# Optimization experiments

Measured on AMD Instinct MI355X. Metric: run time of the kernel, lower is better.

The kernel has to match this reference:

```python
import jax, jax.numpy as jnp
import numpy as np

N_NODES = 100000
N_EDGES = 1600000
D = 128
NEG_SLOPE = 0.01  # torch F.leaky_relu default


def setup_inputs() -> dict:
    key = jax.random.key(0)
    k1, k2, k3, k4, k5, k6 = jax.random.split(key, 6)
    input = jax.random.normal(k1, (N_NODES, D), dtype=jnp.float32)
    edge_row = jax.random.randint(k2, (N_EDGES,), 0, N_NODES, dtype=jnp.int32)
    edge_col = jax.random.randint(k3, (N_EDGES,), 0, N_NODES, dtype=jnp.int32)
    edge_val = jax.random.uniform(k4, (N_EDGES,), dtype=jnp.float32)
    # learned params: W1: Linear(D, D, bias=False), W2: Linear(2D, D, bias=False)
    # torch stores weight as [out, in]; apply as x @ W.T
    bound1 = 1.0 / np.sqrt(D)
    bound2 = 1.0 / np.sqrt(2 * D)
    W1 = jax.random.uniform(k5, (D, D), dtype=jnp.float32, minval=-bound1, maxval=bound1)
    W2 = jax.random.uniform(k6, (D, 2 * D), dtype=jnp.float32, minval=-bound2, maxval=bound2)
    return {"input": input, "edge_row": edge_row, "edge_col": edge_col,
            "edge_val": edge_val, "W1": W1, "W2": W2}


def reference(input, edge_row, edge_col, edge_val, W1, W2):
    # proj_input = W1(input)
    proj = input @ W1.T                                   # [N, D]
    # neighboor = spmm(adj, proj): out[i] = sum_e val[e] * proj[col[e]] for row[e]==i
    msg = edge_val[:, None] * proj[edge_col]              # [E, D]
    neigh = jax.ops.segment_sum(msg, edge_row, num_segments=input.shape[0])  # [N, D]
    h = jnp.concatenate([input + neigh, input * neigh], axis=-1)  # [N, 2D]
    return jax.nn.leaky_relu(h @ W2.T, NEG_SLOPE)         # [N, D]
```

## Files before the change

kernel.cpp:

```cpp
#include <hip/hip_runtime.h>

#define DIM 128
#define BROWS 128
#define BCAP 3072
#define BK_EDGES 2048

typedef __attribute__((ext_vector_type(8))) short short8;
typedef __attribute__((ext_vector_type(4))) float f32x4;

__device__ __forceinline__ unsigned short f2bf(float f) {
    unsigned u = __float_as_uint(f);
    u += 0x7fffu + ((u >> 16) & 1u);
    return (unsigned short)(u >> 16);
}
__device__ __forceinline__ float bf2f(unsigned short b) {
    return __uint_as_float(((unsigned)b) << 16);
}

__global__ void k_pre(const float4* __restrict__ in, const float* __restrict__ W1,
                      const float* __restrict__ W2, unsigned short* __restrict__ inputb,
                      unsigned short* __restrict__ w1b, unsigned short* __restrict__ w2b,
                      int* __restrict__ gcur, int n4, int nCvt, int nbuk) {
    int b = blockIdx.x;
    if (b < nCvt) {
        int i = b * 256 + threadIdx.x;
        if (i < n4) {
            float4 v = in[i];
            *(ushort4*)(inputb + (long)i * 4) =
                make_ushort4(f2bf(v.x), f2bf(v.y), f2bf(v.z), f2bf(v.w));
        }
    } else if (b < nCvt + 192) {
        int idx = (b - nCvt) * 256 + threadIdx.x;
        if (idx < 16384)      w1b[idx] = f2bf(W1[idx]);
        else                  w2b[idx - 16384] = f2bf(W2[idx - 16384]);
    } else {
        int i = (b - nCvt - 192) * 256 + threadIdx.x;
        if (i < nbuk) gcur[i] = 0;
    }
}

__global__ __launch_bounds__(256) void k_bucket(const int* __restrict__ er,
                                                const int* __restrict__ ec,
                                                const float* __restrict__ ev,
                                                int* __restrict__ gcur,
                                                int2* __restrict__ edata, int E, int nbuk) {
    __shared__ int lhist[800];
    __shared__ int lpos[800];
    for (int b = threadIdx.x; b < nbuk; b += 256) lhist[b] = 0;
    __syncthreads();
    int e0 = blockIdx.x * BK_EDGES;
    for (int j = 0; j < BK_EDGES; j += 256) {
        int e = e0 + j + threadIdx.x;
        if (e < E) atomicAdd(&lhist[er[e] >> 7], 1);
    }
    __syncthreads();
    for (int b = threadIdx.x; b < nbuk; b += 256) {
        int c = lhist[b];
        int g = (c > 0) ? atomicAdd(&gcur[b], c) : 0;
        lpos[b] = b * BCAP + g;
    }
    __syncthreads();
    for (int j = 0; j < BK_EDGES; j += 256) {
        int e = e0 + j + threadIdx.x;
        if (e < E) {
            int r = er[e], b = r >> 7;
            int p = atomicAdd(&lpos[b], 1);
            if (p < (b + 1) * BCAP)
                edata[p] = make_int2(((r & 127) << 17) | ec[e], __float_as_int(ev[e]));
        }
    }
}

__global__ __launch_bounds__(256) void k_csr(int2* __restrict__ edata,
                                             const int* __restrict__ gcur,
                                             int* __restrict__ rs, int* __restrict__ re) {
    __shared__ int2 sed[BCAP];
    __shared__ int hist[BROWS];
    __shared__ int scan[BROWS];
    __shared__ int lcur[BROWS];
    int b = blockIdx.x, tid = threadIdx.x;
    int cnt = gcur[b]; if (cnt > BCAP) cnt = BCAP;
    int2* ed = edata + (long)b * BCAP;
    if (tid < BROWS) hist[tid] = 0;
    for (int i = tid; i < cnt; i += 256) sed[i] = ed[i];
    __syncthreads();
    for (int i = tid; i < cnt; i += 256) atomicAdd(&hist[sed[i].x >> 17], 1);
    __syncthreads();
    if (tid < BROWS) scan[tid] = hist[tid];
    __syncthreads();
    for (int off = 1; off < BROWS; off <<= 1) {
        int v = (tid < BROWS && tid >= off) ? scan[tid - off] : 0;
        __syncthreads();
        if (tid < BROWS) scan[tid] += v;
        __syncthreads();
    }
    if (tid < BROWS) {
        int excl = scan[tid] - hist[tid];
        lcur[tid] = excl;
        int row = b * BROWS + tid;
        rs[row] = b * BCAP + excl;
        re[row] = b * BCAP + excl + hist[tid];
    }
    __syncthreads();
    for (int i = tid; i < cnt; i += 256) {
        int2 v = sed[i];
        int p = atomicAdd(&lcur[v.x >> 17], 1);
        ed[p] = make_int2(v.x & 0x1FFFF, v.y);
    }
}

__global__ __launch_bounds__(256) void k_gather(const unsigned short* __restrict__ xb,
                                                const int2* __restrict__ edata,
                                                const int* __restrict__ rs,
                                                const int* __restrict__ re,
                                                unsigned short* __restrict__ aggb, int N) {
    int wave = threadIdx.x >> 6, lane = threadIdx.x & 63;
    int row = blockIdx.x * 4 + wave;
    if (row >= N) return;
    int beg = rs[row], end = re[row];
    float accx = 0.f, accy = 0.f;
    const unsigned* xw = (const unsigned*)xb;
    for (int p = beg; p < end; p += 64) {
        int nc = end - p; if (nc > 64) nc = 64;
        int2 ed = (lane < nc) ? edata[p + lane] : make_int2(0, 0);
        int j = 0;
        for (; j + 4 <= nc; j += 4) {
            int c0 = __shfl(ed.x, j),     c1 = __shfl(ed.x, j + 1);
            int c2 = __shfl(ed.x, j + 2), c3 = __shfl(ed.x, j + 3);
            float v0 = __int_as_float(__shfl(ed.y, j));
            float v1 = __int_as_float(__shfl(ed.y, j + 1));
            float v2 = __int_as_float(__shfl(ed.y, j + 2));
            float v3 = __int_as_float(__shfl(ed.y, j + 3));
            unsigned u0 = xw[(long)c0 * 64 + lane];
            unsigned u1 = xw[(long)c1 * 64 + lane];
            unsigned u2 = xw[(long)c2 * 64 + lane];
            unsigned u3 = xw[(long)c3 * 64 + lane];
            accx += v0 * __uint_as_float(u0 << 16);
            accy += v0 * __uint_as_float(u0 & 0xffff0000u);
            accx += v1 * __uint_as_float(u1 << 16);
            accy += v1 * __uint_as_float(u1 & 0xffff0000u);
            accx += v2 * __uint_as_float(u2 << 16);
            accy += v2 * __uint_as_float(u2 & 0xffff0000u);
            accx += v3 * __uint_as_float(u3 << 16);
            accy += v3 * __uint_as_float(u3 & 0xffff0000u);
        }
        for (; j < nc; ++j) {
            int c = __shfl(ed.x, j);
            float v = __int_as_float(__shfl(ed.y, j));
            unsigned u = xw[(long)c * 64 + lane];
            accx += v * __uint_as_float(u << 16);
            accy += v * __uint_as_float(u & 0xffff0000u);
        }
    }
    *(ushort2*)(aggb + (long)row * DIM + lane * 2) = make_ushort2(f2bf(accx), f2bf(accy));
}

__global__ __launch_bounds__(256, 4) void k_fused(const unsigned short* __restrict__ aggb,
                                                  const unsigned short* __restrict__ inputb,
                                                  const unsigned short* __restrict__ w1b,
                                                  const unsigned short* __restrict__ w2b,
                                                  float* __restrict__ out, int N) {
    __shared__ __align__(16) unsigned short sh[2 * 64 * 136];
    int w = threadIdx.x >> 6, lane = threadIdx.x & 63;
    int quad = lane >> 4, lq = lane & 15;
    int blk0 = blockIdx.x * 64;
    unsigned short* sh0 = sh;
    unsigned short* sh1 = sh + 64 * 136;

    short8 b1[2][4];
#pragma unroll
    for (int ntl = 0; ntl < 2; ++ntl)
#pragma unroll
        for (int kb = 0; kb < 4; ++kb)
            b1[ntl][kb] = *(const short8*)(w1b + ((w * 2 + ntl) * 16 + lq) * DIM +
                                           kb * 32 + quad * 8);

#pragma unroll
    for (int mt = 0; mt < 4; ++mt) {
        short8 afr[4];
        {
            int row = blk0 + mt * 16 + lq; if (row >= N) row = N - 1;
#pragma unroll
            for (int kb = 0; kb < 4; ++kb)
                afr[kb] = *(const short8*)(aggb + (long)row * DIM + kb * 32 + quad * 8);
        }
#pragma unroll
        for (int ntl = 0; ntl < 2; ++ntl) {
            f32x4 c = {0.f, 0.f, 0.f, 0.f};
#pragma unroll
            for (int kb = 0; kb < 4; ++kb)
                c = __builtin_amdgcn_mfma_f32_16x16x32_bf16(afr[kb], b1[ntl][kb], c, 0, 0, 0);
            int nt = w * 2 + ntl;
#pragma unroll
            for (int rg = 0; rg < 4; ++rg) {
                int r = blk0 + mt * 16 + quad * 4 + rg;
                int rr = (r < N) ? r : (N - 1);
                float x = bf2f(inputb[(long)rr * DIM + nt * 16 + lq]);
                float nb = c[rg];
                int off = (mt * 16 + quad * 4 + rg) * 136 + nt * 16 + lq;
                sh0[off] = f2bf(x + nb);
                sh1[off] = f2bf(x * nb);
            }
        }
    }

    short8 b2[2][8];
#pragma unroll
    for (int ntl = 0; ntl < 2; ++ntl)
#pragma unroll
        for (int kb = 0; kb < 8; ++kb)
            b2[ntl][kb] = *(const short8*)(w2b + ((w * 2 + ntl) * 16 + lq) * 256 +
                                           kb * 32 + quad * 8);
    __syncthreads();

#pragma unroll
    for (int mt = 0; mt < 4; ++mt) {
        int arow = (mt * 16 + lq) * 136;
        short8 a0[4], a1[4];
#pragma unroll
        for (int kb = 0; kb < 4; ++kb) {
            a0[kb] = *(const short8*)(sh0 + arow + kb * 32 + quad * 8);
            a1[kb] = *(const short8*)(sh1 + arow + kb * 32 + quad * 8);
        }
#pragma unroll
        for (int ntl = 0; ntl < 2; ++ntl) {
            f32x4 c = {0.f, 0.f, 0.f, 0.f};
#pragma unroll
            for (int kb = 0; kb < 4; ++kb)
                c = __builtin_amdgcn_mfma_f32_16x16x32_bf16(a0[kb], b2[ntl][kb], c, 0, 0, 0);
#pragma unroll
            for (int kb = 0; kb < 4; ++kb)
                c = __builtin_amdgcn_mfma_f32_16x16x32_bf16(a1[kb], b2[ntl][kb + 4], c, 0, 0, 0);
            int nt = w * 2 + ntl;
#pragma unroll
            for (int rg = 0; rg < 4; ++rg) {
                int r = blk0 + mt * 16 + quad * 4 + rg;
                if (r < N) {
                    float v = c[rg];
                    v = (v > 0.f) ? v : 0.01f * v;
                    out[(long)r * DIM + nt * 16 + lq] = v;
                }
            }
        }
    }
}

extern "C" void kernel_launch(void* const* d_in, const int* in_sizes, int n_in,
                              void* d_out, int out_size, void* d_ws, size_t ws_size,
                              hipStream_t stream) {
    const float* input = (const float*)d_in[0];
    const int*   er    = (const int*)d_in[1];
    const int*   ec    = (const int*)d_in[2];
    const float* ev    = (const float*)d_in[3];
    const float* W1    = (const float*)d_in[4];
    const float* W2    = (const float*)d_in[5];
    int N = in_sizes[0] / DIM;
    int E = in_sizes[1];
    float* out = (float*)d_out;
    int nbuk = (N + BROWS - 1) / BROWS;

    int* ws = (int*)d_ws;
    int* gcur = ws;
    int2* edata = (int2*)(ws + 1024);
    int* rs = (int*)(edata + (long)nbuk * BCAP);
    int* re = rs + (long)nbuk * BROWS;
    unsigned short* w1b = (unsigned short*)(re + (long)nbuk * BROWS);
    unsigned short* w2b = w1b + 16384;
    unsigned short* inputb = w2b + 32768;
    unsigned short* aggb = inputb + (long)N * DIM;

    int n4 = N * (DIM / 4);
    int nCvt = (n4 + 255) / 256;
    int nZero = (nbuk + 255) / 256;
    k_pre<<<nCvt + 192 + nZero, 256, 0, stream>>>(
        (const float4*)input, W1, W2, inputb, w1b, w2b, gcur, n4, nCvt, nbuk);

    k_bucket<<<(E + BK_EDGES - 1) / BK_EDGES, 256, 0, stream>>>(
        er, ec, ev, gcur, edata, E, nbuk);

    k_csr<<<nbuk, 256, 0, stream>>>(edata, gcur, rs, re);

    k_gather<<<(N + 3) / 4, 256, 0, stream>>>(inputb, edata, rs, re, aggb, N);

    k_fused<<<(N + 63) / 64, 256, 0, stream>>>(aggb, inputb, w1b, w2b, out, N);
}
```

Measured before the change: 279.9 us.

## Split gather wave into 8 edge groups with 16-byte loads and shuffle reduction

The per-row gather now splits each 64-lane wave into 8 groups of 8 lanes. Each group handles a different edge and loads the full bf16 row with two 16-byte vector loads per lane, instead of one 4-byte load per lane over edges processed one after another. Partial sums are combined with xor-shuffles at the end, and one group writes the result with vector stores. This is meant to raise memory-level parallelism and cut per-edge shuffle overhead. In exchange it uses more registers, adds a reduction step, and leaves groups idle on rows with few or non-multiple-of-8 edges.

```diff
diff --git a/kernel.cpp b/kernel.cpp
--- a/kernel.cpp
+++ b/kernel.cpp
@@ -118,41 +118,46 @@
     int row = blockIdx.x * 4 + wave;
     if (row >= N) return;
     int beg = rs[row], end = re[row];
-    float accx = 0.f, accy = 0.f;
-    const unsigned* xw = (const unsigned*)xb;
-    for (int p = beg; p < end; p += 64) {
-        int nc = end - p; if (nc > 64) nc = 64;
-        int2 ed = (lane < nc) ? edata[p + lane] : make_int2(0, 0);
-        int j = 0;
-        for (; j + 4 <= nc; j += 4) {
-            int c0 = __shfl(ed.x, j),     c1 = __shfl(ed.x, j + 1);
-            int c2 = __shfl(ed.x, j + 2), c3 = __shfl(ed.x, j + 3);
-            float v0 = __int_as_float(__shfl(ed.y, j));
-            float v1 = __int_as_float(__shfl(ed.y, j + 1));
-            float v2 = __int_as_float(__shfl(ed.y, j + 2));
-            float v3 = __int_as_float(__shfl(ed.y, j + 3));
-            unsigned u0 = xw[(long)c0 * 64 + lane];
-            unsigned u1 = xw[(long)c1 * 64 + lane];
-            unsigned u2 = xw[(long)c2 * 64 + lane];
-            unsigned u3 = xw[(long)c3 * 64 + lane];
-            accx += v0 * __uint_as_float(u0 << 16);
-            accy += v0 * __uint_as_float(u0 & 0xffff0000u);
-            accx += v1 * __uint_as_float(u1 << 16);
-            accy += v1 * __uint_as_float(u1 & 0xffff0000u);
-            accx += v2 * __uint_as_float(u2 << 16);
-            accy += v2 * __uint_as_float(u2 & 0xffff0000u);
-            accx += v3 * __uint_as_float(u3 << 16);
-            accy += v3 * __uint_as_float(u3 & 0xffff0000u);
-        }
-        for (; j < nc; ++j) {
-            int c = __shfl(ed.x, j);
-            float v = __int_as_float(__shfl(ed.y, j));
-            unsigned u = xw[(long)c * 64 + lane];
-            accx += v * __uint_as_float(u << 16);
-            accy += v * __uint_as_float(u & 0xffff0000u);
-        }
-    }
-    *(ushort2*)(aggb + (long)row * DIM + lane * 2) = make_ushort2(f2bf(accx), f2bf(accy));
+    int g = lane >> 3, s = lane & 7;
+    float pa[8], pb[8];
+#pragma unroll
+    for (int k = 0; k < 8; ++k) { pa[k] = 0.f; pb[k] = 0.f; }
+    const int4* x4 = (const int4*)xb;
+    for (int p = beg; p < end; p += 8) {
+        int idx = p + g;
+        int2 e = (idx < end) ? edata[idx] : make_int2(0, 0);
+        float v = __int_as_float(e.y);
+        long base = (long)e.x * 16;
+        int4 ua = x4[base + s];
+        int4 ub = x4[base + 8 + s];
+        const unsigned* wa = (const unsigned*)&ua;
+        const unsigned* wb = (const unsigned*)&ub;
+#pragma unroll
+        for (int k = 0; k < 4; ++k) {
+            pa[2 * k]     += v * __uint_as_float(wa[k] << 16);
+            pa[2 * k + 1] += v * __uint_as_float(wa[k] & 0xffff0000u);
+            pb[2 * k]     += v * __uint_as_float(wb[k] << 16);
+            pb[2 * k + 1] += v * __uint_as_float(wb[k] & 0xffff0000u);
+        }
+    }
+#pragma unroll
+    for (int m = 8; m <= 32; m <<= 1) {
+#pragma unroll
+        for (int k = 0; k < 8; ++k) {
+            pa[k] += __shfl_xor(pa[k], m);
+            pb[k] += __shfl_xor(pb[k], m);
+        }
+    }
+    if (g == 0) {
+        short8 oa, ob;
+#pragma unroll
+        for (int k = 0; k < 8; ++k) {
+            oa[k] = (short)f2bf(pa[k]);
+            ob[k] = (short)f2bf(pb[k]);
+        }
+        *(short8*)(aggb + (long)row * DIM + s * 8)      = oa;
+        *(short8*)(aggb + (long)row * DIM + 64 + s * 8) = ob;
+    }
 }
 
 __global__ __launch_bounds__(256, 4) void k_fused(const unsigned short* __restrict__ aggb,
```

After: 280.3 us. About the same (+0.1%).
